# Performance work log

Measured on AMD Instinct MI355X. Metric: run time of the kernel, lower is better.

Reference implementation:

```python
import jax, jax.numpy as jnp
import numpy as np

N, E, F, H, C, ED = 10000, 160000, 4, 32, 4, 2  # nodes, edges, in_feat, hidden, classes, edge_dim


def _init(key, shape, fan_in):
    return jax.random.normal(key, shape, jnp.float32) / np.float32(np.sqrt(fan_in))


def setup_inputs() -> dict:
    key = jax.random.key(0)
    ks = iter(jax.random.split(key, 40))
    inp = {
        "x": jax.random.normal(next(ks), (N, F), jnp.float32),
        "edge_index": jax.random.randint(next(ks), (2, E), 0, N, dtype=jnp.int32),
        "edge_attr": jax.random.normal(next(ks), (E, ED), jnp.float32),
    }
    for i, din in enumerate([F, H, H]):
        inp[f"w1_{i}"] = _init(next(ks), (ED, H), ED)
        inp[f"b1_{i}"] = jnp.zeros((H,), jnp.float32)
        inp[f"w2_{i}"] = _init(next(ks), (H, din * H), H)
        inp[f"b2_{i}"] = jnp.zeros((din * H,), jnp.float32)
        inp[f"root_{i}"] = _init(next(ks), (din, H), din)
        inp[f"bias_{i}"] = jnp.zeros((H,), jnp.float32)
    inp["fc_w"] = _init(next(ks), (H, C), H)
    inp["fc_b"] = jnp.zeros((C,), jnp.float32)
    return inp


def _nnconv(x, src, dst, edge_attr, w1, b1, w2, b2, root, bias):
    # edge MLP -> per-edge weight matrix [E, din, H]
    h = jax.nn.relu(edge_attr @ w1 + b1)                      # [E, H]
    W = (h @ w2 + b2).reshape(E, x.shape[1], -1)              # [E, din, H]
    msg = jnp.einsum('ei,eio->eo', x[src], W)                 # gather + per-edge matvec
    agg = jax.ops.segment_sum(msg, dst, num_segments=N)       # scatter-add to targets
    return agg + x @ root + bias                              # root weight + bias (NNConv)


def reference(x, edge_index, edge_attr,
              w1_0, b1_0, w2_0, b2_0, root_0, bias_0,
              w1_1, b1_1, w2_1, b2_1, root_1, bias_1,
              w1_2, b1_2, w2_2, b2_2, root_2, bias_2,
              fc_w, fc_b):
    src, dst = edge_index[0], edge_index[1]
    layers = [(w1_0, b1_0, w2_0, b2_0, root_0, bias_0),
              (w1_1, b1_1, w2_1, b2_1, root_1, bias_1),
              (w1_2, b1_2, w2_2, b2_2, root_2, bias_2)]
    for p in layers:
        x = jax.nn.relu(_nnconv(x, src, dst, edge_attr, *p))  # dropout=0 -> no-op
    logits = x @ fc_w + fc_b
    return jax.nn.log_softmax(logits, axis=1)
```

## Files before the change

### kernel.cpp

```cpp
#include <hip/hip_runtime.h>
#include <hip/hip_bf16.h>
#include <math.h>

#define N_NODES 10000
#define N_EDGES 160000

typedef __attribute__((ext_vector_type(8))) short bf16x8;
typedef __attribute__((ext_vector_type(4))) float f32x4;
typedef __attribute__((ext_vector_type(4))) double f64x4;

static __device__ inline unsigned short f2b(float v) {
    __hip_bfloat16 b = __float2bfloat16(v);
    return *reinterpret_cast<unsigned short*>(&b);
}

__global__ __launch_bounds__(256) void k_tw2z(const float* __restrict__ s0,
                                              const float* __restrict__ s1,
                                              const float* __restrict__ s2,
                                              float* __restrict__ t0,
                                              float* __restrict__ t1,
                                              float* __restrict__ t2,
                                              int* __restrict__ cntz) {
    int tid = blockIdx.x * 256 + threadIdx.x;
    if (tid < 20480) { cntz[tid] = 0; return; }
    int d = tid - 20480;
    if (d < 4096) {
        int i = d >> 10, j = d & 1023, o = j >> 5, k = j & 31;
        t0[d] = s0[k * 128 + i * 32 + o];
    } else if (d < 4096 + 32768) {
        int q = d - 4096;
        int i = q >> 10, j = q & 1023, o = j >> 5, k = j & 31;
        t1[q] = s1[k * 1024 + i * 32 + o];
    } else if (d < 4096 + 65536) {
        int q = d - 4096 - 32768;
        int i = q >> 10, j = q & 1023, o = j >> 5, k = j & 31;
        t2[q] = s2[k * 1024 + i * 32 + o];
    }
}

__global__ __launch_bounds__(256) void k_hist2(const int* __restrict__ ei,
                                               int* __restrict__ cnt,
                                               int* __restrict__ cntd) {
    int e = blockIdx.x * 256 + threadIdx.x;
    if (e < N_EDGES) {
        atomicAdd(&cnt[ei[e]], 1);
        atomicAdd(&cntd[ei[N_EDGES + e]], 1);
    }
}

__global__ __launch_bounds__(256) void k_scan2(const int* __restrict__ cnt,
                                               const int* __restrict__ cntd,
                                               int* __restrict__ off,
                                               int* __restrict__ dst_off,
                                               int* __restrict__ cursor,
                                               int* __restrict__ cursord) {
    const int* c; int* o; int* cu;
    if (blockIdx.x == 0) { c = cnt;  o = off;     cu = cursor;  }
    else                 { c = cntd; o = dst_off; cu = cursord; }
    __shared__ int part[256];
    int t = threadIdx.x;
    int base = t * 40;
    int s = 0;
    for (int i = 0; i < 40; ++i) {
        int idx = base + i;
        if (idx < N_NODES) s += c[idx];
    }
    part[t] = s;
    __syncthreads();
    for (int d = 1; d < 256; d <<= 1) {
        int v = (t >= d) ? part[t - d] : 0;
        __syncthreads();
        part[t] += v;
        __syncthreads();
    }
    int run = part[t] - s;
    for (int i = 0; i < 40; ++i) {
        int idx = base + i;
        if (idx < N_NODES) {
            o[idx] = run;
            cu[idx] = run;
            run += c[idx];
        }
    }
    if (t == 255) o[N_NODES] = run;
}

__global__ __launch_bounds__(256) void k_scatter(const int* __restrict__ ei,
                                                 const float* __restrict__ ea,
                                                 int* __restrict__ cursor,
                                                 int* __restrict__ cursord,
                                                 int* __restrict__ qmap,
                                                 float* __restrict__ ea_s) {
    int e = blockIdx.x * 256 + threadIdx.x;
    if (e >= N_EDGES) return;
    float a0 = ea[2 * e], a1 = ea[2 * e + 1];
    int src = ei[e], dst = ei[N_EDGES + e];
    int pos = atomicAdd(&cursor[src], 1);
    int q   = atomicAdd(&cursord[dst], 1);
    qmap[pos] = q;
    *(float2*)(ea_s + 2 * (size_t)pos) = make_float2(a0, a1);
}

template <int DIN, bool FIRST>
__global__ __launch_bounds__(256) void k_G(const float* __restrict__ xin,
                                           const int* __restrict__ dst_off,
                                           const float* __restrict__ msgd,
                                           const float* __restrict__ w2t,
                                           const float* __restrict__ b2,
                                           const float* __restrict__ root,
                                           const float* __restrict__ bias,
                                           unsigned short* __restrict__ Gb,
                                           float* __restrict__ xb2,
                                           float* __restrict__ agg) {
    const int t = threadIdx.x;
    const int n0 = blockIdx.x * 8;

    __shared__ float xs[8 * DIN];
    if constexpr (FIRST) {
        for (int idx = t; idx < 8 * DIN; idx += 256) {
            int m = idx / DIN, i = idx - m * DIN;
            xs[idx] = xin[(size_t)(n0 + m) * DIN + i];
        }
        __syncthreads();
    } else {
        __shared__ f64x4 part[256];
        {
            int m = t >> 5, s = t & 31;
            int g = s >> 2, quar = s & 3;
            int n = n0 + m;
            int jb = dst_off[n], je = dst_off[n + 1];
            f64x4 a0 = {0.0, 0.0, 0.0, 0.0}, a1 = {0.0, 0.0, 0.0, 0.0};
            int j = jb + quar;
            for (; j + 4 < je; j += 8) {
                f32x4 m0 = *(const f32x4*)(msgd + (size_t)j * 32 + g * 4);
                f32x4 m1 = *(const f32x4*)(msgd + (size_t)(j + 4) * 32 + g * 4);
                a0 += __builtin_convertvector(m0, f64x4);
                a1 += __builtin_convertvector(m1, f64x4);
            }
            if (j < je) {
                f32x4 m0 = *(const f32x4*)(msgd + (size_t)j * 32 + g * 4);
                a0 += __builtin_convertvector(m0, f64x4);
            }
            part[t] = a0 + a1;
        }
        __syncthreads();
        if (t < 64) {
            int m = t >> 3, g = t & 7;
            f64x4 v = part[m * 32 + g * 4] + part[m * 32 + g * 4 + 1] +
                      part[m * 32 + g * 4 + 2] + part[m * 32 + g * 4 + 3];
            const f32x4 xi = *(const f32x4*)(xin + (size_t)(n0 + m) * 32 + g * 4);
            v += __builtin_convertvector(xi, f64x4);
#pragma unroll
            for (int c = 0; c < 4; ++c) {
                float f = (float)v[c];
                xs[m * 32 + g * 4 + c] = f > 0.f ? f : 0.f;
            }
        }
        __syncthreads();
    }

    float acc[8][4];
#pragma unroll
    for (int m = 0; m < 8; ++m)
        acc[m][0] = acc[m][1] = acc[m][2] = acc[m][3] = 0.f;

#pragma unroll
    for (int i = 0; i < DIN; ++i) {
        const float4 w = *(const float4*)(w2t + i * 1024 + t * 4);
#pragma unroll
        for (int m = 0; m < 8; ++m) {
            float xv = xs[m * DIN + i];
            acc[m][0] += xv * w.x;
            acc[m][1] += xv * w.y;
            acc[m][2] += xv * w.z;
            acc[m][3] += xv * w.w;
        }
    }
#pragma unroll
    for (int m = 0; m < 8; ++m) {
        unsigned int p0 = (unsigned int)f2b(acc[m][0]) | ((unsigned int)f2b(acc[m][1]) << 16);
        unsigned int p1 = (unsigned int)f2b(acc[m][2]) | ((unsigned int)f2b(acc[m][3]) << 16);
        *(uint2*)(Gb + (size_t)(n0 + m) * 1024 + t * 4) = make_uint2(p0, p1);
    }

    {
        int m = t >> 5, o = t & 31;
        float ab = 0.f, ar = bias[o];
#pragma unroll
        for (int i = 0; i < DIN; ++i) {
            float xv = xs[m * DIN + i];
            ab += xv * b2[i * 32 + o];
            ar += xv * root[i * 32 + o];
        }
        size_t p = (size_t)(n0 + m) * 32 + o;
        xb2[p] = ab;
        agg[p] = ar;
    }
}

__global__ __launch_bounds__(256) void k_edge(const int* __restrict__ off,
                                              const int* __restrict__ qmap,
                                              const float* __restrict__ ea_s,
                                              const float* __restrict__ w1,
                                              const float* __restrict__ b1,
                                              const unsigned short* __restrict__ Gb,
                                              const float* __restrict__ xb2,
                                              float* __restrict__ msgd) {
    int t = threadIdx.x;
    int lane = t & 63;
    int n = blockIdx.x * 4 + (t >> 6);
    int col = lane & 15;
    int quad = lane >> 4;

    float wa[8], wb[8], bb[8];
#pragma unroll
    for (int j = 0; j < 8; ++j) {
        int o = quad * 8 + j;
        wa[j] = w1[o];
        wb[j] = w1[32 + o];
        bb[j] = b1[o];
    }

    const bf16x8 b_lo = *(const bf16x8*)(Gb + (size_t)n * 1024 + col * 32 + quad * 8);
    const bf16x8 b_hi = *(const bf16x8*)(Gb + (size_t)n * 1024 + (col + 16) * 32 + quad * 8);
    float xb_lo = xb2[(size_t)n * 32 + col];
    float xb_hi = xb2[(size_t)n * 32 + 16 + col];

    int jb = off[n], je = off[n + 1];
    for (int e0 = jb; e0 < je; e0 += 16) {
        int eA = e0 + col;
        bf16x8 afrag = {0, 0, 0, 0, 0, 0, 0, 0};
        if (eA < je) {
            float2 a = *(const float2*)(ea_s + 2 * (size_t)eA);
            union { unsigned int u[4]; bf16x8 v; } cv;
#pragma unroll
            for (int j = 0; j < 4; ++j) {
                float v0 = fmaxf(a.x * wa[2 * j]     + a.y * wb[2 * j]     + bb[2 * j],     0.f);
                float v1 = fmaxf(a.x * wa[2 * j + 1] + a.y * wb[2 * j + 1] + bb[2 * j + 1], 0.f);
                cv.u[j] = (unsigned int)f2b(v0) | ((unsigned int)f2b(v1) << 16);
            }
            afrag = cv.v;
        }
        f32x4 acc_lo = {xb_lo, xb_lo, xb_lo, xb_lo};
        f32x4 acc_hi = {xb_hi, xb_hi, xb_hi, xb_hi};
        acc_lo = __builtin_amdgcn_mfma_f32_16x16x32_bf16(afrag, b_lo, acc_lo, 0, 0, 0);
        acc_hi = __builtin_amdgcn_mfma_f32_16x16x32_bf16(afrag, b_hi, acc_hi, 0, 0, 0);
#pragma unroll
        for (int r = 0; r < 4; ++r) {
            int er = e0 + quad * 4 + r;
            if (er < je) {
                int q = qmap[er];
                msgd[(size_t)q * 32 + col] = acc_lo[r];
                msgd[(size_t)q * 32 + 16 + col] = acc_hi[r];
            }
        }
    }
}

__global__ __launch_bounds__(256) void k_final(const float* __restrict__ agg,
                                               const int* __restrict__ dst_off,
                                               const float* __restrict__ msgd,
                                               const float* __restrict__ fcw,
                                               const float* __restrict__ fcb,
                                               float* __restrict__ out) {
    __shared__ f64x4 part[256];
    __shared__ float xs[8 * 32];
    int t = threadIdx.x;
    {
        int m = t >> 5, s = t & 31;
        int g = s >> 2, quar = s & 3;
        int n = blockIdx.x * 8 + m;
        int jb = dst_off[n], je = dst_off[n + 1];
        f64x4 a0 = {0.0, 0.0, 0.0, 0.0}, a1 = {0.0, 0.0, 0.0, 0.0};
        int j = jb + quar;
        for (; j + 4 < je; j += 8) {
            f32x4 m0 = *(const f32x4*)(msgd + (size_t)j * 32 + g * 4);
            f32x4 m1 = *(const f32x4*)(msgd + (size_t)(j + 4) * 32 + g * 4);
            a0 += __builtin_convertvector(m0, f64x4);
            a1 += __builtin_convertvector(m1, f64x4);
        }
        if (j < je) {
            f32x4 m0 = *(const f32x4*)(msgd + (size_t)j * 32 + g * 4);
            a0 += __builtin_convertvector(m0, f64x4);
        }
        part[t] = a0 + a1;
    }
    __syncthreads();
    if (t < 64) {
        int m = t >> 3, g = t & 7;
        f64x4 v = part[m * 32 + g * 4] + part[m * 32 + g * 4 + 1] +
                  part[m * 32 + g * 4 + 2] + part[m * 32 + g * 4 + 3];
        int n = blockIdx.x * 8 + m;
        const f32x4 ag = *(const f32x4*)(agg + (size_t)n * 32 + g * 4);
        v += __builtin_convertvector(ag, f64x4);
#pragma unroll
        for (int c = 0; c < 4; ++c) {
            float f = (float)v[c];
            xs[m * 32 + g * 4 + c] = f > 0.f ? f : 0.f;
        }
    }
    __syncthreads();
    if (t < 8) {
        int nn = blockIdx.x * 8 + t;
        float l0 = fcb[0], l1 = fcb[1], l2 = fcb[2], l3 = fcb[3];
#pragma unroll
        for (int oo = 0; oo < 32; ++oo) {
            float xv = xs[t * 32 + oo];
            l0 += xv * fcw[oo * 4 + 0];
            l1 += xv * fcw[oo * 4 + 1];
            l2 += xv * fcw[oo * 4 + 2];
            l3 += xv * fcw[oo * 4 + 3];
        }
        float mx = fmaxf(fmaxf(l0, l1), fmaxf(l2, l3));
        float s = expf(l0 - mx) + expf(l1 - mx) + expf(l2 - mx) + expf(l3 - mx);
        float lse = mx + logf(s);
        out[(size_t)nn * 4 + 0] = l0 - lse;
        out[(size_t)nn * 4 + 1] = l1 - lse;
        out[(size_t)nn * 4 + 2] = l2 - lse;
        out[(size_t)nn * 4 + 3] = l3 - lse;
    }
}

extern "C" void kernel_launch(void* const* d_in, const int* in_sizes, int n_in,
                              void* d_out, int out_size, void* d_ws, size_t ws_size,
                              hipStream_t stream) {
    const float* x0 = (const float*)d_in[0];
    const int*   ei = (const int*)d_in[1];
    const float* ea = (const float*)d_in[2];
    const float *W1[3], *B1[3], *W2[3], *B2[3], *RT[3], *BS[3];
    for (int l = 0; l < 3; ++l) {
        W1[l] = (const float*)d_in[3 + 6 * l];
        B1[l] = (const float*)d_in[4 + 6 * l];
        W2[l] = (const float*)d_in[5 + 6 * l];
        B2[l] = (const float*)d_in[6 + 6 * l];
        RT[l] = (const float*)d_in[7 + 6 * l];
        BS[l] = (const float*)d_in[8 + 6 * l];
    }
    const float* fcw = (const float*)d_in[21];
    const float* fcb = (const float*)d_in[22];
    float* out = (float*)d_out;

    int*   cnt     = (int*)d_ws;
    int*   cntd    = cnt + 10240;
    int*   cursor  = cntd + 10240;
    int*   cursord = cursor + 10240;
    int*   off     = cursord + 10240;
    int*   dst_off = off + 10240;
    int*   qmap    = dst_off + 10240;
    float* w2t0    = (float*)(qmap + 160000);
    float* w2t1    = w2t0 + 4096;
    float* w2t2    = w2t1 + 32768;
    float* xb2     = w2t2 + 32768;
    float* aggA    = xb2 + 320000;
    float* aggB    = aggA + 320000;
    float* msgd    = aggB + 320000;
    float* ea_s    = msgd + 5120000;
    unsigned short* Gb = (unsigned short*)(ea_s + 320000);

    const int gE256 = (N_EDGES + 255) / 256;
    const int gG    = N_NODES / 8;
    const int gEdge = N_NODES / 4;

    k_tw2z<<<352, 256, 0, stream>>>(W2[0], W2[1], W2[2], w2t0, w2t1, w2t2, cnt);
    k_hist2<<<gE256, 256, 0, stream>>>(ei, cnt, cntd);
    k_scan2<<<2, 256, 0, stream>>>(cnt, cntd, off, dst_off, cursor, cursord);
    k_scatter<<<gE256, 256, 0, stream>>>(ei, ea, cursor, cursord, qmap, ea_s);

    k_G<4, true><<<gG, 256, 0, stream>>>(x0, dst_off, msgd, w2t0, B2[0], RT[0], BS[0], Gb, xb2, aggA);
    k_edge<<<gEdge, 256, 0, stream>>>(off, qmap, ea_s, W1[0], B1[0], Gb, xb2, msgd);

    k_G<32, false><<<gG, 256, 0, stream>>>(aggA, dst_off, msgd, w2t1, B2[1], RT[1], BS[1], Gb, xb2, aggB);
    k_edge<<<gEdge, 256, 0, stream>>>(off, qmap, ea_s, W1[1], B1[1], Gb, xb2, msgd);

    k_G<32, false><<<gG, 256, 0, stream>>>(aggB, dst_off, msgd, w2t2, B2[2], RT[2], BS[2], Gb, xb2, aggA);
    k_edge<<<gEdge, 256, 0, stream>>>(off, qmap, ea_s, W1[2], B1[2], Gb, xb2, msgd);

    k_final<<<(N_NODES + 7) / 8, 256, 0, stream>>>(aggA, dst_off, msgd, fcw, fcb, out);
}
```

Measured before the change: 257.4 us.

## Fuse pipeline into persistent megakernel with software grid barriers

After: 910.2 us. 254% more time.

```diff
diff --git a/kernel.cpp b/kernel.cpp
--- a/kernel.cpp
+++ b/kernel.cpp
@@ -4,6 +4,7 @@
 
 #define N_NODES 10000
 #define N_EDGES 160000
+#define NBLK 512
 
 typedef __attribute__((ext_vector_type(8))) short bf16x8;
 typedef __attribute__((ext_vector_type(4))) float f32x4;
@@ -14,16 +15,16 @@
     return *reinterpret_cast<unsigned short*>(&b);
 }
 
-__global__ __launch_bounds__(256) void k_tw2z(const float* __restrict__ s0,
-                                              const float* __restrict__ s1,
-                                              const float* __restrict__ s2,
-                                              float* __restrict__ t0,
-                                              float* __restrict__ t1,
-                                              float* __restrict__ t2,
-                                              int* __restrict__ cntz) {
+__global__ __launch_bounds__(256) void k_pre(const float* __restrict__ s0,
+                                             const float* __restrict__ s1,
+                                             const float* __restrict__ s2,
+                                             float* __restrict__ t0,
+                                             float* __restrict__ t1,
+                                             float* __restrict__ t2,
+                                             int* __restrict__ z) {
     int tid = blockIdx.x * 256 + threadIdx.x;
-    if (tid < 20480) { cntz[tid] = 0; return; }
-    int d = tid - 20480;
+    if (tid < 21760) { z[tid] = 0; return; }
+    int d = tid - 21760;
     if (d < 4096) {
         int i = d >> 10, j = d & 1023, o = j >> 5, k = j & 31;
         t0[d] = s0[k * 128 + i * 32 + o];
@@ -38,26 +39,37 @@
     }
 }
 
-__global__ __launch_bounds__(256) void k_hist2(const int* __restrict__ ei,
-                                               int* __restrict__ cnt,
-                                               int* __restrict__ cntd) {
-    int e = blockIdx.x * 256 + threadIdx.x;
-    if (e < N_EDGES) {
-        atomicAdd(&cnt[ei[e]], 1);
-        atomicAdd(&cntd[ei[N_EDGES + e]], 1);
-    }
-}
-
-__global__ __launch_bounds__(256) void k_scan2(const int* __restrict__ cnt,
-                                               const int* __restrict__ cntd,
-                                               int* __restrict__ off,
-                                               int* __restrict__ dst_off,
-                                               int* __restrict__ cursor,
-                                               int* __restrict__ cursord) {
-    const int* c; int* o; int* cu;
-    if (blockIdx.x == 0) { c = cnt;  o = off;     cu = cursor;  }
-    else                 { c = cntd; o = dst_off; cu = cursord; }
-    __shared__ int part[256];
+__device__ __forceinline__ void grid_sync(int* flags, int* genp, int it) {
+    __syncthreads();
+    const int t = threadIdx.x;
+    if (blockIdx.x == 0) {
+        for (int b = t; b < NBLK; b += 256) {
+            if (b == 0) continue;
+            while (__hip_atomic_load(&flags[b], __ATOMIC_RELAXED, __HIP_MEMORY_SCOPE_AGENT) < it)
+                __builtin_amdgcn_s_sleep(2);
+        }
+        __syncthreads();
+        if (t == 0) {
+            __threadfence();
+            __hip_atomic_store(genp, it, __ATOMIC_RELEASE, __HIP_MEMORY_SCOPE_AGENT);
+        }
+        __syncthreads();
+    } else {
+        if (t == 0) {
+            __threadfence();
+            __hip_atomic_store(&flags[blockIdx.x], it, __ATOMIC_RELEASE, __HIP_MEMORY_SCOPE_AGENT);
+            while (__hip_atomic_load(genp, __ATOMIC_RELAXED, __HIP_MEMORY_SCOPE_AGENT) < it)
+                __builtin_amdgcn_s_sleep(2);
+            __threadfence();
+        }
+        __syncthreads();
+    }
+}
+
+
+__device__ void scan_body(const int* __restrict__ c, int* __restrict__ o, int* __restrict__ cu,
+                          char* smem) {
+    int* part = (int*)smem;
     int t = threadIdx.x;
     int base = t * 40;
     int s = 0;
@@ -83,39 +95,25 @@
         }
     }
     if (t == 255) o[N_NODES] = run;
-}
-
-__global__ __launch_bounds__(256) void k_scatter(const int* __restrict__ ei,
-                                                 const float* __restrict__ ea,
-                                                 int* __restrict__ cursor,
-                                                 int* __restrict__ cursord,
-                                                 int* __restrict__ qmap,
-                                                 float* __restrict__ ea_s) {
-    int e = blockIdx.x * 256 + threadIdx.x;
-    if (e >= N_EDGES) return;
-    float a0 = ea[2 * e], a1 = ea[2 * e + 1];
-    int src = ei[e], dst = ei[N_EDGES + e];
-    int pos = atomicAdd(&cursor[src], 1);
-    int q   = atomicAdd(&cursord[dst], 1);
-    qmap[pos] = q;
-    *(float2*)(ea_s + 2 * (size_t)pos) = make_float2(a0, a1);
+    __syncthreads();
 }
 
 template <int DIN, bool FIRST>
-__global__ __launch_bounds__(256) void k_G(const float* __restrict__ xin,
-                                           const int* __restrict__ dst_off,
-                                           const float* __restrict__ msgd,
-                                           const float* __restrict__ w2t,
-                                           const float* __restrict__ b2,
-                                           const float* __restrict__ root,
-                                           const float* __restrict__ bias,
-                                           unsigned short* __restrict__ Gb,
-                                           float* __restrict__ xb2,
-                                           float* __restrict__ agg) {
+__device__ __forceinline__ void G_unit(int n0,
+                                       const float* __restrict__ xin,
+                                       const int* __restrict__ dst_off,
+                                       const float* __restrict__ msgd,
+                                       const float* __restrict__ w2t,
+                                       const float* __restrict__ b2,
+                                       const float* __restrict__ root,
+                                       const float* __restrict__ bias,
+                                       unsigned short* __restrict__ Gb,
+                                       float* __restrict__ xb2,
+                                       float* __restrict__ agg,
+                                       char* smem) {
     const int t = threadIdx.x;
-    const int n0 = blockIdx.x * 8;
-
-    __shared__ float xs[8 * DIN];
+    float* xs = (float*)(smem + 8192);
+
     if constexpr (FIRST) {
         for (int idx = t; idx < 8 * DIN; idx += 256) {
             int m = idx / DIN, i = idx - m * DIN;
@@ -123,7 +121,7 @@
         }
         __syncthreads();
     } else {
-        __shared__ f64x4 part[256];
+        f64x4* part = (f64x4*)smem;
         {
             int m = t >> 5, s = t & 31;
             int g = s >> 2, quar = s & 3;
@@ -196,31 +194,17 @@
         xb2[p] = ab;
         agg[p] = ar;
     }
-}
-
-__global__ __launch_bounds__(256) void k_edge(const int* __restrict__ off,
-                                              const int* __restrict__ qmap,
-                                              const float* __restrict__ ea_s,
-                                              const float* __restrict__ w1,
-                                              const float* __restrict__ b1,
-                                              const unsigned short* __restrict__ Gb,
-                                              const float* __restrict__ xb2,
-                                              float* __restrict__ msgd) {
-    int t = threadIdx.x;
-    int lane = t & 63;
-    int n = blockIdx.x * 4 + (t >> 6);
-    int col = lane & 15;
-    int quad = lane >> 4;
-
-    float wa[8], wb[8], bb[8];
-#pragma unroll
-    for (int j = 0; j < 8; ++j) {
-        int o = quad * 8 + j;
-        wa[j] = w1[o];
-        wb[j] = w1[32 + o];
-        bb[j] = b1[o];
-    }
-
+    __syncthreads();
+}
+
+__device__ __forceinline__ void edge_node(int n, int col, int quad,
+                                          const float* wa, const float* wb, const float* bb,
+                                          const int* __restrict__ off,
+                                          const int* __restrict__ qmap,
+                                          const float* __restrict__ ea_s,
+                                          const unsigned short* __restrict__ Gb,
+                                          const float* __restrict__ xb2,
+                                          float* __restrict__ msgd) {
     const bf16x8 b_lo = *(const bf16x8*)(Gb + (size_t)n * 1024 + col * 32 + quad * 8);
     const bf16x8 b_hi = *(const bf16x8*)(Gb + (size_t)n * 1024 + (col + 16) * 32 + quad * 8);
     float xb_lo = xb2[(size_t)n * 32 + col];
@@ -257,19 +241,44 @@
     }
 }
 
-__global__ __launch_bounds__(256) void k_final(const float* __restrict__ agg,
-                                               const int* __restrict__ dst_off,
-                                               const float* __restrict__ msgd,
-                                               const float* __restrict__ fcw,
-                                               const float* __restrict__ fcb,
-                                               float* __restrict__ out) {
-    __shared__ f64x4 part[256];
-    __shared__ float xs[8 * 32];
+__device__ __forceinline__ void edge_phase(const int* __restrict__ off,
+                                           const int* __restrict__ qmap,
+                                           const float* __restrict__ ea_s,
+                                           const float* __restrict__ w1,
+                                           const float* __restrict__ b1,
+                                           const unsigned short* __restrict__ Gb,
+                                           const float* __restrict__ xb2,
+                                           float* __restrict__ msgd) {
+    const int t = threadIdx.x;
+    int lane = t & 63, wave = t >> 6;
+    int col = lane & 15, quad = lane >> 4;
+    float wa[8], wb[8], bb[8];
+#pragma unroll
+    for (int j = 0; j < 8; ++j) {
+        int o = quad * 8 + j;
+        wa[j] = w1[o];
+        wb[j] = w1[32 + o];
+        bb[j] = b1[o];
+    }
+    for (int u = blockIdx.x; u < 2500; u += NBLK)
+        edge_node(u * 4 + wave, col, quad, wa, wb, bb, off, qmap, ea_s, Gb, xb2, msgd);
+}
+
+__device__ __forceinline__ void final_unit(int n0,
+                                           const float* __restrict__ agg,
+                                           const int* __restrict__ dst_off,
+                                           const float* __restrict__ msgd,
+                                           const float* __restrict__ fcw,
+                                           const float* __restrict__ fcb,
+                                           float* __restrict__ out,
+                                           char* smem) {
+    f64x4* part = (f64x4*)smem;
+    float* xs = (float*)(smem + 8192);
     int t = threadIdx.x;
     {
         int m = t >> 5, s = t & 31;
         int g = s >> 2, quar = s & 3;
-        int n = blockIdx.x * 8 + m;
+        int n = n0 + m;
         int jb = dst_off[n], je = dst_off[n + 1];
         f64x4 a0 = {0.0, 0.0, 0.0, 0.0}, a1 = {0.0, 0.0, 0.0, 0.0};
         int j = jb + quar;
@@ -290,7 +299,7 @@
         int m = t >> 3, g = t & 7;
         f64x4 v = part[m * 32 + g * 4] + part[m * 32 + g * 4 + 1] +
                   part[m * 32 + g * 4 + 2] + part[m * 32 + g * 4 + 3];
-        int n = blockIdx.x * 8 + m;
+        int n = n0 + m;
         const f32x4 ag = *(const f32x4*)(agg + (size_t)n * 32 + g * 4);
         v += __builtin_convertvector(ag, f64x4);
 #pragma unroll
@@ -301,7 +310,7 @@
     }
     __syncthreads();
     if (t < 8) {
-        int nn = blockIdx.x * 8 + t;
+        int nn = n0 + t;
         float l0 = fcb[0], l1 = fcb[1], l2 = fcb[2], l3 = fcb[3];
 #pragma unroll
         for (int oo = 0; oo < 32; ++oo) {
@@ -319,6 +328,73 @@
         out[(size_t)nn * 4 + 2] = l2 - lse;
         out[(size_t)nn * 4 + 3] = l3 - lse;
     }
+    __syncthreads();
+}
+
+__global__ __launch_bounds__(256, 4) void k_mega(
+        const int* __restrict__ ei, const float* __restrict__ ea, const float* __restrict__ x0,
+        const float* __restrict__ w1a, const float* __restrict__ b1a,
+        const float* __restrict__ w1b, const float* __restrict__ b1b,
+        const float* __restrict__ w1c, const float* __restrict__ b1c,
+        const float* __restrict__ w2t0, const float* __restrict__ w2t1, const float* __restrict__ w2t2,
+        const float* __restrict__ b2a, const float* __restrict__ b2b, const float* __restrict__ b2c,
+        const float* __restrict__ rta, const float* __restrict__ rtb, const float* __restrict__ rtc,
+        const float* __restrict__ bsa, const float* __restrict__ bsb, const float* __restrict__ bsc,
+        const float* __restrict__ fcw, const float* __restrict__ fcb,
+        int* cnt, int* cntd, int* cursor, int* cursord, int* off, int* dst_off, int* qmap,
+        float* ea_s, float* xb2, float* aggA, float* aggB, float* msgd,
+        unsigned short* Gb, int* bar, float* out) {
+    __shared__ __align__(32) char smem[9216];
+    const int t = threadIdx.x;
+    const int bid = blockIdx.x;
+    int* flags = bar;
+    int* genp = bar + 1024;
+
+    for (int u = bid; u < 625; u += NBLK) {
+        int e = u * 256 + t;
+        atomicAdd(&cnt[ei[e]], 1);
+        atomicAdd(&cntd[ei[N_EDGES + e]], 1);
+    }
+    grid_sync(flags, genp, 1);
+
+    if (bid == 0) scan_body(cnt, off, cursor, smem);
+    else if (bid == 1) scan_body(cntd, dst_off, cursord, smem);
+    grid_sync(flags, genp, 2);
+
+    for (int u = bid; u < 1875; u += NBLK) {
+        if (u < 1250) {
+            G_unit<4, true>(u * 8, x0, dst_off, msgd, w2t0, b2a, rta, bsa, Gb, xb2, aggA, smem);
+        } else {
+            int e = (u - 1250) * 256 + t;
+            float a0 = ea[2 * e], a1 = ea[2 * e + 1];
+            int src = ei[e], dst = ei[N_EDGES + e];
+            int pos = atomicAdd(&cursor[src], 1);
+            int q = atomicAdd(&cursord[dst], 1);
+            qmap[pos] = q;
+            *(float2*)(ea_s + 2 * (size_t)pos) = make_float2(a0, a1);
+        }
+    }
+    grid_sync(flags, genp, 3);
+
+    edge_phase(off, qmap, ea_s, w1a, b1a, Gb, xb2, msgd);
+    grid_sync(flags, genp, 4);
+
+    for (int u = bid; u < 1250; u += NBLK)
+        G_unit<32, false>(u * 8, aggA, dst_off, msgd, w2t1, b2b, rtb, bsb, Gb, xb2, aggB, smem);
+    grid_sync(flags, genp, 5);
+
+    edge_phase(off, qmap, ea_s, w1b, b1b, Gb, xb2, msgd);
+    grid_sync(flags, genp, 6);
+
+    for (int u = bid; u < 1250; u += NBLK)
+        G_unit<32, false>(u * 8, aggB, dst_off, msgd, w2t2, b2c, rtc, bsc, Gb, xb2, aggA, smem);
+    grid_sync(flags, genp, 7);
+
+    edge_phase(off, qmap, ea_s, w1c, b1c, Gb, xb2, msgd);
+    grid_sync(flags, genp, 8);
+
+    for (int u = bid; u < 1250; u += NBLK)
+        final_unit(u * 8, aggA, dst_off, msgd, fcw, fcb, out, smem);
 }
 
 extern "C" void kernel_launch(void* const* d_in, const int* in_sizes, int n_in,
@@ -342,7 +418,8 @@
 
     int*   cnt     = (int*)d_ws;
     int*   cntd    = cnt + 10240;
-    int*   cursor  = cntd + 10240;
+    int*   bar     = cntd + 10240;
+    int*   cursor  = bar + 1280;
     int*   cursord = cursor + 10240;
     int*   off     = cursord + 10240;
     int*   dst_off = off + 10240;
@@ -357,23 +434,15 @@
     float* ea_s    = msgd + 5120000;
     unsigned short* Gb = (unsigned short*)(ea_s + 320000);
 
-    const int gE256 = (N_EDGES + 255) / 256;
-    const int gG    = N_NODES / 8;
-    const int gEdge = N_NODES / 4;
-
-    k_tw2z<<<352, 256, 0, stream>>>(W2[0], W2[1], W2[2], w2t0, w2t1, w2t2, cnt);
-    k_hist2<<<gE256, 256, 0, stream>>>(ei, cnt, cntd);
-    k_scan2<<<2, 256, 0, stream>>>(cnt, cntd, off, dst_off, cursor, cursord);
-    k_scatter<<<gE256, 256, 0, stream>>>(ei, ea, cursor, cursord, qmap, ea_s);
-
-    k_G<4, true><<<gG, 256, 0, stream>>>(x0, dst_off, msgd, w2t0, B2[0], RT[0], BS[0], Gb, xb2, aggA);
-    k_edge<<<gEdge, 256, 0, stream>>>(off, qmap, ea_s, W1[0], B1[0], Gb, xb2, msgd);
-
-    k_G<32, false><<<gG, 256, 0, stream>>>(aggA, dst_off, msgd, w2t1, B2[1], RT[1], BS[1], Gb, xb2, aggB);
-    k_edge<<<gEdge, 256, 0, stream>>>(off, qmap, ea_s, W1[1], B1[1], Gb, xb2, msgd);
-
-    k_G<32, false><<<gG, 256, 0, stream>>>(aggB, dst_off, msgd, w2t2, B2[2], RT[2], BS[2], Gb, xb2, aggA);
-    k_edge<<<gEdge, 256, 0, stream>>>(off, qmap, ea_s, W1[2], B1[2], Gb, xb2, msgd);
-
-    k_final<<<(N_NODES + 7) / 8, 256, 0, stream>>>(aggA, dst_off, msgd, fcw, fcb, out);
-}
+    k_pre<<<357, 256, 0, stream>>>(W2[0], W2[1], W2[2], w2t0, w2t1, w2t2, cnt);
+    k_mega<<<NBLK, 256, 0, stream>>>(ei, ea, x0,
+                                     W1[0], B1[0], W1[1], B1[1], W1[2], B1[2],
+                                     w2t0, w2t1, w2t2,
+                                     B2[0], B2[1], B2[2],
+                                     RT[0], RT[1], RT[2],
+                                     BS[0], BS[1], BS[2],
+                                     fcw, fcb,
+                                     cnt, cntd, cursor, cursord, off, dst_off, qmap,
+                                     ea_s, xb2, aggA, aggB, msgd,
+                                     Gb, bar, out);
+}
```
